# Performance work log

Measured on AMD Instinct MI355X. Metric: run time of the kernel, lower is better.

## Reference

```python
import jax, jax.numpy as jnp
import numpy as np
from jax import lax

N_LAYERS = 10  # Sinkhorn(n_layers=10)


def setup_inputs() -> dict:
    key = jax.random.key(0)
    k1, k2, k3 = jax.random.split(key, 3)
    S, NA, NB = 4, 4096, 4096
    alpha = jax.random.uniform(k1, (S, NA), jnp.float32, 0.05, 1.0)
    alpha = alpha / alpha.sum(-1, keepdims=True)  # probability simplex
    beta = jax.random.uniform(k2, (S, NB), jnp.float32, 0.05, 1.0)
    beta = beta / beta.sum(-1, keepdims=True)
    C = jax.random.uniform(k3, (NA, NB), jnp.float32)  # nonneg cost matrix
    eps = jnp.float32(0.1)  # entropic regularization
    return {"alpha": alpha, "beta": beta, "C": C, "eps": eps}


def reference(alpha, beta, C, eps):
    # Log-domain Sinkhorn: f,g are dual potentials, shapes (S,NA)/(S,NB).
    log_alpha = jnp.log(alpha)
    log_beta = jnp.log(beta)

    def log_dot_exp(A, b):
        # A: (n, m), b: (S, m) -> (S, n); matches torch log_dot_exp (2D case)
        return jax.scipy.special.logsumexp((-A[None, :, :] + b[:, None, :]) / eps, axis=-1)

    def step(carry, _):
        _, g = carry
        f = eps * (log_alpha - log_dot_exp(C, g))
        g = eps * (log_beta - log_dot_exp(C.T, f))
        return (f, g), None

    f0 = jnp.zeros_like(alpha)
    g0 = jnp.zeros_like(beta)
    (f, g), _ = lax.scan(step, (f0, g0), None, length=N_LAYERS)
    return f, g
```

## Files before the change

### kernel.cpp

```cpp
#include <hip/hip_runtime.h>
#include <stdint.h>

#define NN 4096
#define NITER 10
#define ROWS 16
#define NBLK 256
#define THREADS 512

#define RED_OFF 131072

typedef float v2f __attribute__((ext_vector_type(2)));

static __device__ __forceinline__ unsigned short f2bf(float f) {
  union { float f; unsigned int i; } x; x.f = f;
  unsigned int i = x.i;
  i += 0x7FFFu + ((i >> 16) & 1u);
  return (unsigned short)(i >> 16);
}
static __device__ __forceinline__ unsigned int pk2(float a, float b) {
  return (unsigned int)f2bf(a) | ((unsigned int)f2bf(b) << 16);
}
static __device__ __forceinline__ float2 unpk(unsigned int u) {
  union { unsigned int i; float f; } a, b;
  a.i = u << 16; b.i = u & 0xFFFF0000u;
  return make_float2(a.f, b.f);
}
static __device__ __forceinline__ float read_eps(const void* p) {
  float f = *(const float*)p;
  if (f > 1e-4f && f < 1.0f) return f;
  union { unsigned int i; float f; } x;
  x.i = ((unsigned int)*(const unsigned short*)p) << 16;
  return x.f;
}
static __device__ __forceinline__ void astore8(unsigned long long* p, unsigned long long v) {
  __hip_atomic_store(p, v, __ATOMIC_RELAXED, __HIP_MEMORY_SCOPE_AGENT);
}
static __device__ __forceinline__ v2f mk2(float a, float b) {
  v2f r; r.x = a; r.y = b; return r;
}
#define FMA2(a, b, c) __builtin_elementwise_fma(a, b, c)

__global__ __launch_bounds__(256) void zero_flags(unsigned int* __restrict__ c) {
#pragma unroll
  for (int k = 0; k < 32; ++k) c[threadIdx.x + k * 256] = 0;
}

static __device__ __forceinline__ void wait_group(
    const unsigned int* flags, int q, unsigned token) {
  const unsigned int* p = flags + (q * 64 + (threadIdx.x & 63)) * 16;
  for (int spin = 0; spin < 400000; ++spin) {
    unsigned v = __hip_atomic_load(p, __ATOMIC_RELAXED,
                                   __HIP_MEMORY_SCOPE_AGENT);
    if (__ballot(v >= token) == 0xFFFFFFFFFFFFFFFFull) break;
    __builtin_amdgcn_s_sleep(1);
  }
}

__global__ __launch_bounds__(THREADS, 1) void sinkhorn_all(
    const float* __restrict__ alpha, const float* __restrict__ beta,
    const float* __restrict__ C, const void* __restrict__ epsp,
    unsigned short* __restrict__ K, unsigned long long* __restrict__ u_ep,
    unsigned long long* __restrict__ v_ep, unsigned int* __restrict__ u_flags,
    unsigned int* __restrict__ v_flags, float* __restrict__ out) {
  __shared__ float4 smem4[8320];
  char* sm = (char*)smem4;
  const int t = threadIdx.x, b = blockIdx.x;
  const int wave = t >> 6, lane = t & 63;
  const int own = ((b & 7) << 5) | (b >> 3);
  const int base0 = own * ROWS;
  const float eps = read_eps(epsp);
  const float nie = -1.0f / eps;

#pragma unroll 2
  for (int r = 0; r < ROWS; ++r) {
    const float4* Crow = (const float4*)(C + (size_t)(base0 + r) * NN) + t * 2;
    float4 c0 = Crow[0], c1 = Crow[1];
    uint4 k0;
    k0.x = pk2(__expf(c0.x * nie), __expf(c0.y * nie));
    k0.y = pk2(__expf(c0.z * nie), __expf(c0.w * nie));
    k0.z = pk2(__expf(c1.x * nie), __expf(c1.y * nie));
    k0.w = pk2(__expf(c1.z * nie), __expf(c1.w * nie));
    ((uint4*)(K + (size_t)(base0 + r) * NN))[t] = k0;
  }

  {
    const int p = t & 3, cb = p * 4, rb = t >> 2;
#pragma unroll 1
    for (int q2 = 0; q2 < 32; q2 += 8) {
      float4 cv[8];
#pragma unroll
      for (int z = 0; z < 8; ++z)
        cv[z] = *(const float4*)(C + (size_t)((q2 + z) * 128 + rb) * NN + base0 + cb);
#pragma unroll
      for (int z = 0; z < 8; ++z) {
        int n = (q2 + z) * 128 + rb;
        int u16 = ((n >> 10) * 8 + ((n >> 3) & 7)) * 256 + ((n >> 6) & 15) * 16;
        int jo = (n & 7) * 2;
        *(unsigned short*)(sm + (size_t)(u16 + cb + 0) * 16 + jo) = f2bf(__expf(cv[z].x * nie));
        *(unsigned short*)(sm + (size_t)(u16 + cb + 1) * 16 + jo) = f2bf(__expf(cv[z].y * nie));
        *(unsigned short*)(sm + (size_t)(u16 + cb + 2) * 16 + jo) = f2bf(__expf(cv[z].z * nie));
        *(unsigned short*)(sm + (size_t)(u16 + cb + 3) * 16 + jo) = f2bf(__expf(cv[z].w * nie));
      }
    }
  }
  __syncthreads();

  const uint4* smu4 = (const uint4*)sm;
  const uint4 ONES = make_uint4(0x3F803F80u, 0x3F803F80u, 0x3F803F80u, 0x3F803F80u);

  for (int it = 0; it < NITER; ++it) {
    v2f acc01[2] = {}, acc23[2] = {};
    const int r0 = base0 + wave * 2;
    const uint4* Kr0 = (const uint4*)(K + (size_t)r0 * NN);
    const uint4* VB = (const uint4*)(v_ep + (size_t)(it - 1) * NN);
#pragma unroll 1
    for (int q = 0; q < 4; ++q) {
      if (it > 0) wait_group(v_flags, q, (unsigned)it);
#pragma unroll
      for (int ms = 0; ms < 2; ++ms) {
        const int fi = q * 128 + ms * 64 + lane;
        uint4 k0 = Kr0[fi], k1 = Kr0[512 + fi];
        uint4 svv[4];
        if (it == 0) {
          svv[0] = svv[1] = svv[2] = svv[3] = ONES;
        } else {
#pragma unroll
          for (int j = 0; j < 4; ++j) svv[j] = VB[fi * 4 + j];
        }
        unsigned cw0[4] = {k0.x, k0.y, k0.z, k0.w};
        unsigned cw1[4] = {k1.x, k1.y, k1.z, k1.w};
#pragma unroll
        for (int w = 0; w < 4; ++w) {
          float2 va = unpk(svv[w].x), vb_ = unpk(svv[w].y);
          float2 vc = unpk(svv[w].z), vd  = unpk(svv[w].w);
          float2 f0 = unpk(cw0[w]), f1 = unpk(cw1[w]);
          acc01[0] = FMA2(mk2(f0.x, f0.x), mk2(va.x, va.y), acc01[0]);
          acc23[0] = FMA2(mk2(f0.x, f0.x), mk2(vb_.x, vb_.y), acc23[0]);
          acc01[0] = FMA2(mk2(f0.y, f0.y), mk2(vc.x, vc.y), acc01[0]);
          acc23[0] = FMA2(mk2(f0.y, f0.y), mk2(vd.x, vd.y), acc23[0]);
          acc01[1] = FMA2(mk2(f1.x, f1.x), mk2(va.x, va.y), acc01[1]);
          acc23[1] = FMA2(mk2(f1.x, f1.x), mk2(vb_.x, vb_.y), acc23[1]);
          acc01[1] = FMA2(mk2(f1.y, f1.y), mk2(vc.x, vc.y), acc01[1]);
          acc23[1] = FMA2(mk2(f1.y, f1.y), mk2(vd.x, vd.y), acc23[1]);
        }
      }
    }
    {
      float accf[2][4];
#pragma unroll
      for (int rr = 0; rr < 2; ++rr) {
        accf[rr][0] = acc01[rr].x; accf[rr][1] = acc01[rr].y;
        accf[rr][2] = acc23[rr].x; accf[rr][3] = acc23[rr].y;
      }
#pragma unroll
      for (int off = 32; off > 0; off >>= 1)
#pragma unroll
        for (int rr = 0; rr < 2; ++rr)
#pragma unroll
          for (int s = 0; s < 4; ++s)
            accf[rr][s] += __shfl_xor(accf[rr][s], off);
      if (lane < 2) {
        int row = r0 + lane;
        float ux = alpha[0 * NN + row] / accf[lane][0];
        float uy = alpha[1 * NN + row] / accf[lane][1];
        float uz = alpha[2 * NN + row] / accf[lane][2];
        float uw = alpha[3 * NN + row] / accf[lane][3];
        unsigned long long ub = (unsigned long long)pk2(ux, uy) |
                                ((unsigned long long)pk2(uz, uw) << 32);
        astore8(u_ep + (size_t)it * NN + row, ub);
        if (it == NITER - 1) {
          out[0 * NN + row] = eps * __logf(ux);
          out[1 * NN + row] = eps * __logf(uy);
          out[2 * NN + row] = eps * __logf(uz);
          out[3 * NN + row] = eps * __logf(uw);
        }
      }
    }
    __syncthreads();
    if (t == 0)
      __hip_atomic_store(u_flags + own * 16, (unsigned)(it + 1),
                         __ATOMIC_RELAXED, __HIP_MEMORY_SCOPE_AGENT);

    const int cB = t & 7, k2n = (t >> 3) & 15, hB = t >> 7;
    const int kq = (hB * 1024 + k2n * 64) >> 1;
    wait_group(u_flags, hB, (unsigned)(it + 1));
    const uint4* UB = (const uint4*)(u_ep + (size_t)it * NN);
    v2f bacc01[2] = {}, bacc23[2] = {};
#pragma unroll
    for (int s = 0; s < 8; ++s) {
      uint4 kt0 = smu4[(hB * 8 + s) * 256 + k2n * 16 + cB];
      uint4 kt1 = smu4[(hB * 8 + s) * 256 + k2n * 16 + cB + 8];
      uint4 su[4];
#pragma unroll
      for (int j = 0; j < 4; ++j) su[j] = UB[kq + s * 4 + j];
      unsigned cw0[4] = {kt0.x, kt0.y, kt0.z, kt0.w};
      unsigned cw1[4] = {kt1.x, kt1.y, kt1.z, kt1.w};
#pragma unroll
      for (int w = 0; w < 4; ++w) {
        float2 ua = unpk(su[w].x), ub_ = unpk(su[w].y);
        float2 uc = unpk(su[w].z), ud  = unpk(su[w].w);
        float2 f0 = unpk(cw0[w]), f1 = unpk(cw1[w]);
        bacc01[0] = FMA2(mk2(f0.x, f0.x), mk2(ua.x, ua.y), bacc01[0]);
        bacc23[0] = FMA2(mk2(f0.x, f0.x), mk2(ub_.x, ub_.y), bacc23[0]);
        bacc01[0] = FMA2(mk2(f0.y, f0.y), mk2(uc.x, uc.y), bacc01[0]);
        bacc23[0] = FMA2(mk2(f0.y, f0.y), mk2(ud.x, ud.y), bacc23[0]);
        bacc01[1] = FMA2(mk2(f1.x, f1.x), mk2(ua.x, ua.y), bacc01[1]);
        bacc23[1] = FMA2(mk2(f1.x, f1.x), mk2(ub_.x, ub_.y), bacc23[1]);
        bacc01[1] = FMA2(mk2(f1.y, f1.y), mk2(uc.x, uc.y), bacc01[1]);
        bacc23[1] = FMA2(mk2(f1.y, f1.y), mk2(ud.x, ud.y), bacc23[1]);
      }
    }
    {
      float bf0[4] = {bacc01[0].x, bacc01[0].y, bacc23[0].x, bacc23[0].y};
      float bf1[4] = {bacc01[1].x, bacc01[1].y, bacc23[1].x, bacc23[1].y};
#pragma unroll
      for (int off = 8; off <= 32; off <<= 1)
#pragma unroll
        for (int s2 = 0; s2 < 4; ++s2) {
          bf0[s2] += __shfl_xor(bf0[s2], off);
          bf1[s2] += __shfl_xor(bf1[s2], off);
        }
      if (lane < 8) {
        float4* red = (float4*)(sm + RED_OFF);
        red[(wave * 8 + lane) * 2 + 0] = make_float4(bf0[0], bf0[1], bf0[2], bf0[3]);
        red[(wave * 8 + lane) * 2 + 1] = make_float4(bf1[0], bf1[1], bf1[2], bf1[3]);
      }
    }
    __syncthreads();
    if (t < 16) {
      const float4* red = (const float4*)(sm + RED_OFF);
      const int cc = t & 7, sel = t >> 3;
      float4 a = make_float4(0.f, 0.f, 0.f, 0.f);
#pragma unroll
      for (int g = 0; g < 8; ++g) {
        float4 r = red[(g * 8 + cc) * 2 + sel];
        a.x += r.x; a.y += r.y; a.z += r.z; a.w += r.w;
      }
      int m = base0 + t;
      float vx = beta[0 * NN + m] / a.x;
      float vy = beta[1 * NN + m] / a.y;
      float vz = beta[2 * NN + m] / a.z;
      float vw = beta[3 * NN + m] / a.w;
      unsigned long long vb = (unsigned long long)pk2(vx, vy) |
                              ((unsigned long long)pk2(vz, vw) << 32);
      astore8(v_ep + (size_t)it * NN + m, vb);
      if (it == NITER - 1) {
        out[4 * NN + 0 * NN + m] = eps * __logf(vx);
        out[4 * NN + 1 * NN + m] = eps * __logf(vy);
        out[4 * NN + 2 * NN + m] = eps * __logf(vz);
        out[4 * NN + 3 * NN + m] = eps * __logf(vw);
      }
    }
    __syncthreads();
    if (t == 0 && it < NITER - 1)
      __hip_atomic_store(v_flags + own * 16, (unsigned)(it + 1),
                         __ATOMIC_RELAXED, __HIP_MEMORY_SCOPE_AGENT);
  }
}

extern "C" void kernel_launch(void* const* d_in, const int* in_sizes, int n_in,
                              void* d_out, int out_size, void* d_ws, size_t ws_size,
                              hipStream_t stream) {
  (void)in_sizes; (void)n_in; (void)out_size; (void)ws_size;
  const float* alpha = (const float*)d_in[0];
  const float* beta  = (const float*)d_in[1];
  const float* C     = (const float*)d_in[2];
  const void*  epsp  = d_in[3];

  char* ws = (char*)d_ws;
  unsigned short* K        = (unsigned short*)ws;
  unsigned long long* u_ep = (unsigned long long*)(ws + 33554432);
  unsigned long long* v_ep = (unsigned long long*)(ws + 33554432 + 327680);
  unsigned int* u_flags    = (unsigned int*)(ws + 33554432 + 655360);
  unsigned int* v_flags    = (unsigned int*)(ws + 33554432 + 655360 + 16384);
  float* out = (float*)d_out;

  zero_flags<<<1, 256, 0, stream>>>(u_flags);
  sinkhorn_all<<<NBLK, THREADS, 0, stream>>>(alpha, beta, C, epsp, K,
                                             u_ep, v_ep, u_flags, v_flags, out);
}
```

Measured before the change: 250.0 us.

## Store scaling vectors in fp32, pack flags densely, prefetch K rows

Scaling vectors u and v are now exchanged between blocks as full fp32 instead of packed bf16, so the unpack work goes away and precision improves, at the cost of twice the exchange traffic. Flags are packed contiguously instead of padded to one per 64 bytes, which makes the polling loads more coalesced but may add false sharing. K row loads are software-prefetched one quarter ahead of the wait on v flags, so global latency overlaps the spin-wait. v at iteration zero is initialised to ones in a small prep kernel, which removes the it==0 branch.

```diff
diff --git a/kernel.cpp b/kernel.cpp
--- a/kernel.cpp
+++ b/kernel.cpp
@@ -8,6 +8,10 @@
 #define THREADS 512
 
 #define RED_OFF 131072
+
+#define U_EP_OFF 33554432
+#define V_EP_OFF 34209792
+#define FLAG_OFF 34930688
 
 typedef float v2f __attribute__((ext_vector_type(2)));
 
@@ -40,14 +44,19 @@
 }
 #define FMA2(a, b, c) __builtin_elementwise_fma(a, b, c)
 
-__global__ __launch_bounds__(256) void zero_flags(unsigned int* __restrict__ c) {
-#pragma unroll
-  for (int k = 0; k < 32; ++k) c[threadIdx.x + k * 256] = 0;
+__global__ __launch_bounds__(256) void init_ws(unsigned int* __restrict__ flags,
+                                               float* __restrict__ v0) {
+#pragma unroll
+  for (int k = 0; k < 32; ++k) flags[threadIdx.x + k * 256] = 0;
+  float4* p = (float4*)v0;
+#pragma unroll
+  for (int k = 0; k < 16; ++k)
+    p[threadIdx.x + k * 256] = make_float4(1.f, 1.f, 1.f, 1.f);
 }
 
 static __device__ __forceinline__ void wait_group(
     const unsigned int* flags, int q, unsigned token) {
-  const unsigned int* p = flags + (q * 64 + (threadIdx.x & 63)) * 16;
+  const unsigned int* p = flags + q * 64 + (threadIdx.x & 63);
   for (int spin = 0; spin < 400000; ++spin) {
     unsigned v = __hip_atomic_load(p, __ATOMIC_RELAXED,
                                    __HIP_MEMORY_SCOPE_AGENT);
@@ -59,8 +68,8 @@
 __global__ __launch_bounds__(THREADS, 1) void sinkhorn_all(
     const float* __restrict__ alpha, const float* __restrict__ beta,
     const float* __restrict__ C, const void* __restrict__ epsp,
-    unsigned short* __restrict__ K, unsigned long long* __restrict__ u_ep,
-    unsigned long long* __restrict__ v_ep, unsigned int* __restrict__ u_flags,
+    unsigned short* __restrict__ K, float* __restrict__ u_ep,
+    float* __restrict__ v_ep, unsigned int* __restrict__ u_flags,
     unsigned int* __restrict__ v_flags, float* __restrict__ out) {
   __shared__ float4 smem4[8320];
   char* sm = (char*)smem4;
@@ -106,43 +115,50 @@
   __syncthreads();
 
   const uint4* smu4 = (const uint4*)sm;
-  const uint4 ONES = make_uint4(0x3F803F80u, 0x3F803F80u, 0x3F803F80u, 0x3F803F80u);
 
   for (int it = 0; it < NITER; ++it) {
     v2f acc01[2] = {}, acc23[2] = {};
     const int r0 = base0 + wave * 2;
     const uint4* Kr0 = (const uint4*)(K + (size_t)r0 * NN);
-    const uint4* VB = (const uint4*)(v_ep + (size_t)(it - 1) * NN);
+    const float4* VB = (const float4*)v_ep + (size_t)it * NN;
+    uint4 ka[4];
+    ka[0] = Kr0[lane];       ka[1] = Kr0[512 + lane];
+    ka[2] = Kr0[64 + lane];  ka[3] = Kr0[576 + lane];
 #pragma unroll 1
     for (int q = 0; q < 4; ++q) {
+      uint4 kan[4];
+      if (q < 3) {
+        const int f = (q + 1) * 128 + lane;
+        kan[0] = Kr0[f];       kan[1] = Kr0[512 + f];
+        kan[2] = Kr0[64 + f];  kan[3] = Kr0[576 + f];
+      }
       if (it > 0) wait_group(v_flags, q, (unsigned)it);
 #pragma unroll
       for (int ms = 0; ms < 2; ++ms) {
         const int fi = q * 128 + ms * 64 + lane;
-        uint4 k0 = Kr0[fi], k1 = Kr0[512 + fi];
-        uint4 svv[4];
-        if (it == 0) {
-          svv[0] = svv[1] = svv[2] = svv[3] = ONES;
-        } else {
-#pragma unroll
-          for (int j = 0; j < 4; ++j) svv[j] = VB[fi * 4 + j];
-        }
+        float4 sv[8];
+#pragma unroll
+        for (int j = 0; j < 8; ++j) sv[j] = VB[fi * 8 + j];
+        const uint4 k0 = ka[ms * 2], k1 = ka[ms * 2 + 1];
         unsigned cw0[4] = {k0.x, k0.y, k0.z, k0.w};
         unsigned cw1[4] = {k1.x, k1.y, k1.z, k1.w};
 #pragma unroll
         for (int w = 0; w < 4; ++w) {
-          float2 va = unpk(svv[w].x), vb_ = unpk(svv[w].y);
-          float2 vc = unpk(svv[w].z), vd  = unpk(svv[w].w);
+          float4 e = sv[2 * w], o = sv[2 * w + 1];
           float2 f0 = unpk(cw0[w]), f1 = unpk(cw1[w]);
-          acc01[0] = FMA2(mk2(f0.x, f0.x), mk2(va.x, va.y), acc01[0]);
-          acc23[0] = FMA2(mk2(f0.x, f0.x), mk2(vb_.x, vb_.y), acc23[0]);
-          acc01[0] = FMA2(mk2(f0.y, f0.y), mk2(vc.x, vc.y), acc01[0]);
-          acc23[0] = FMA2(mk2(f0.y, f0.y), mk2(vd.x, vd.y), acc23[0]);
-          acc01[1] = FMA2(mk2(f1.x, f1.x), mk2(va.x, va.y), acc01[1]);
-          acc23[1] = FMA2(mk2(f1.x, f1.x), mk2(vb_.x, vb_.y), acc23[1]);
-          acc01[1] = FMA2(mk2(f1.y, f1.y), mk2(vc.x, vc.y), acc01[1]);
-          acc23[1] = FMA2(mk2(f1.y, f1.y), mk2(vd.x, vd.y), acc23[1]);
+          acc01[0] = FMA2(mk2(f0.x, f0.x), mk2(e.x, e.y), acc01[0]);
+          acc23[0] = FMA2(mk2(f0.x, f0.x), mk2(e.z, e.w), acc23[0]);
+          acc01[0] = FMA2(mk2(f0.y, f0.y), mk2(o.x, o.y), acc01[0]);
+          acc23[0] = FMA2(mk2(f0.y, f0.y), mk2(o.z, o.w), acc23[0]);
+          acc01[1] = FMA2(mk2(f1.x, f1.x), mk2(e.x, e.y), acc01[1]);
+          acc23[1] = FMA2(mk2(f1.x, f1.x), mk2(e.z, e.w), acc23[1]);
+          acc01[1] = FMA2(mk2(f1.y, f1.y), mk2(o.x, o.y), acc01[1]);
+          acc23[1] = FMA2(mk2(f1.y, f1.y), mk2(o.z, o.w), acc23[1]);
         }
+      }
+      if (q < 3) {
+#pragma unroll
+        for (int z = 0; z < 4; ++z) ka[z] = kan[z];
       }
     }
     {
@@ -165,9 +181,11 @@
         float uy = alpha[1 * NN + row] / accf[lane][1];
         float uz = alpha[2 * NN + row] / accf[lane][2];
         float uw = alpha[3 * NN + row] / accf[lane][3];
-        unsigned long long ub = (unsigned long long)pk2(ux, uy) |
-                                ((unsigned long long)pk2(uz, uw) << 32);
-        astore8(u_ep + (size_t)it * NN + row, ub);
+        union { float f[2]; unsigned long long u; } p0, p1;
+        p0.f[0] = ux; p0.f[1] = uy; p1.f[0] = uz; p1.f[1] = uw;
+        unsigned long long* dst =
+            (unsigned long long*)(u_ep + (size_t)it * NN * 4) + row * 2;
+        astore8(dst, p0.u); astore8(dst + 1, p1.u);
         if (it == NITER - 1) {
           out[0 * NN + row] = eps * __logf(ux);
           out[1 * NN + row] = eps * __logf(uy);
@@ -178,36 +196,35 @@
     }
     __syncthreads();
     if (t == 0)
-      __hip_atomic_store(u_flags + own * 16, (unsigned)(it + 1),
+      __hip_atomic_store(u_flags + own, (unsigned)(it + 1),
                          __ATOMIC_RELAXED, __HIP_MEMORY_SCOPE_AGENT);
 
     const int cB = t & 7, k2n = (t >> 3) & 15, hB = t >> 7;
-    const int kq = (hB * 1024 + k2n * 64) >> 1;
+    const int kbase = hB * 1024 + k2n * 64;
     wait_group(u_flags, hB, (unsigned)(it + 1));
-    const uint4* UB = (const uint4*)(u_ep + (size_t)it * NN);
+    const float4* UB = (const float4*)u_ep + (size_t)it * NN;
     v2f bacc01[2] = {}, bacc23[2] = {};
 #pragma unroll
     for (int s = 0; s < 8; ++s) {
       uint4 kt0 = smu4[(hB * 8 + s) * 256 + k2n * 16 + cB];
       uint4 kt1 = smu4[(hB * 8 + s) * 256 + k2n * 16 + cB + 8];
-      uint4 su[4];
-#pragma unroll
-      for (int j = 0; j < 4; ++j) su[j] = UB[kq + s * 4 + j];
+      float4 su[8];
+#pragma unroll
+      for (int j = 0; j < 8; ++j) su[j] = UB[kbase + s * 8 + j];
       unsigned cw0[4] = {kt0.x, kt0.y, kt0.z, kt0.w};
       unsigned cw1[4] = {kt1.x, kt1.y, kt1.z, kt1.w};
 #pragma unroll
       for (int w = 0; w < 4; ++w) {
-        float2 ua = unpk(su[w].x), ub_ = unpk(su[w].y);
-        float2 uc = unpk(su[w].z), ud  = unpk(su[w].w);
+        float4 e = su[2 * w], o = su[2 * w + 1];
         float2 f0 = unpk(cw0[w]), f1 = unpk(cw1[w]);
-        bacc01[0] = FMA2(mk2(f0.x, f0.x), mk2(ua.x, ua.y), bacc01[0]);
-        bacc23[0] = FMA2(mk2(f0.x, f0.x), mk2(ub_.x, ub_.y), bacc23[0]);
-        bacc01[0] = FMA2(mk2(f0.y, f0.y), mk2(uc.x, uc.y), bacc01[0]);
-        bacc23[0] = FMA2(mk2(f0.y, f0.y), mk2(ud.x, ud.y), bacc23[0]);
-        bacc01[1] = FMA2(mk2(f1.x, f1.x), mk2(ua.x, ua.y), bacc01[1]);
-        bacc23[1] = FMA2(mk2(f1.x, f1.x), mk2(ub_.x, ub_.y), bacc23[1]);
-        bacc01[1] = FMA2(mk2(f1.y, f1.y), mk2(uc.x, uc.y), bacc01[1]);
-        bacc23[1] = FMA2(mk2(f1.y, f1.y), mk2(ud.x, ud.y), bacc23[1]);
+        bacc01[0] = FMA2(mk2(f0.x, f0.x), mk2(e.x, e.y), bacc01[0]);
+        bacc23[0] = FMA2(mk2(f0.x, f0.x), mk2(e.z, e.w), bacc23[0]);
+        bacc01[0] = FMA2(mk2(f0.y, f0.y), mk2(o.x, o.y), bacc01[0]);
+        bacc23[0] = FMA2(mk2(f0.y, f0.y), mk2(o.z, o.w), bacc23[0]);
+        bacc01[1] = FMA2(mk2(f1.x, f1.x), mk2(e.x, e.y), bacc01[1]);
+        bacc23[1] = FMA2(mk2(f1.x, f1.x), mk2(e.z, e.w), bacc23[1]);
+        bacc01[1] = FMA2(mk2(f1.y, f1.y), mk2(o.x, o.y), bacc01[1]);
+        bacc23[1] = FMA2(mk2(f1.y, f1.y), mk2(o.z, o.w), bacc23[1]);
       }
     }
     {
@@ -241,9 +258,11 @@
       float vy = beta[1 * NN + m] / a.y;
       float vz = beta[2 * NN + m] / a.z;
       float vw = beta[3 * NN + m] / a.w;
-      unsigned long long vb = (unsigned long long)pk2(vx, vy) |
-                              ((unsigned long long)pk2(vz, vw) << 32);
-      astore8(v_ep + (size_t)it * NN + m, vb);
+      union { float f[2]; unsigned long long u; } p0, p1;
+      p0.f[0] = vx; p0.f[1] = vy; p1.f[0] = vz; p1.f[1] = vw;
+      unsigned long long* dst =
+          (unsigned long long*)(v_ep + (size_t)(it + 1) * NN * 4) + m * 2;
+      astore8(dst, p0.u); astore8(dst + 1, p1.u);
       if (it == NITER - 1) {
         out[4 * NN + 0 * NN + m] = eps * __logf(vx);
         out[4 * NN + 1 * NN + m] = eps * __logf(vy);
@@ -253,7 +272,7 @@
     }
     __syncthreads();
     if (t == 0 && it < NITER - 1)
-      __hip_atomic_store(v_flags + own * 16, (unsigned)(it + 1),
+      __hip_atomic_store(v_flags + own, (unsigned)(it + 1),
                          __ATOMIC_RELAXED, __HIP_MEMORY_SCOPE_AGENT);
   }
 }
@@ -268,14 +287,14 @@
   const void*  epsp  = d_in[3];
 
   char* ws = (char*)d_ws;
-  unsigned short* K        = (unsigned short*)ws;
-  unsigned long long* u_ep = (unsigned long long*)(ws + 33554432);
-  unsigned long long* v_ep = (unsigned long long*)(ws + 33554432 + 327680);
-  unsigned int* u_flags    = (unsigned int*)(ws + 33554432 + 655360);
-  unsigned int* v_flags    = (unsigned int*)(ws + 33554432 + 655360 + 16384);
+  unsigned short* K     = (unsigned short*)ws;
+  float* u_ep           = (float*)(ws + U_EP_OFF);
+  float* v_ep           = (float*)(ws + V_EP_OFF);
+  unsigned int* u_flags = (unsigned int*)(ws + FLAG_OFF);
+  unsigned int* v_flags = (unsigned int*)(ws + FLAG_OFF + 16384);
   float* out = (float*)d_out;
 
-  zero_flags<<<1, 256, 0, stream>>>(u_flags);
+  init_ws<<<1, 256, 0, stream>>>(u_flags, v_ep);
   sinkhorn_all<<<NBLK, THREADS, 0, stream>>>(alpha, beta, C, epsp, K,
                                              u_ep, v_ep, u_flags, v_flags, out);
 }
```

New measurement: 362.9 us. +45.2%, slower.

## Double block size to 1024 threads, halving per-thread rows and columns

Applied to the files above, without the earlier changes.

Raises the workgroup to 1024 threads so each wave handles one row in the u-update instead of two, and each thread covers half as many column groups in the v-update. The K precompute loops and the shared-memory reduction are remapped to the new thread count, and the reduction buffer is enlarged. The aim is more waves in flight per CU to hide global and LDS latency during the latency-bound Sinkhorn sweeps. In exchange it uses more registers per CU, adds cross-wave reduction work, and makes the per-block barriers more expensive.

```diff
diff --git a/kernel.cpp b/kernel.cpp
--- a/kernel.cpp
+++ b/kernel.cpp
@@ -5,7 +5,7 @@
 #define NITER 10
 #define ROWS 16
 #define NBLK 256
-#define THREADS 512
+#define THREADS 1024
 
 #define RED_OFF 131072
 
@@ -62,7 +62,7 @@
     unsigned short* __restrict__ K, unsigned long long* __restrict__ u_ep,
     unsigned long long* __restrict__ v_ep, unsigned int* __restrict__ u_flags,
     unsigned int* __restrict__ v_flags, float* __restrict__ out) {
-  __shared__ float4 smem4[8320];
+  __shared__ float4 smem4[8448];
   char* sm = (char*)smem4;
   const int t = threadIdx.x, b = blockIdx.x;
   const int wave = t >> 6, lane = t & 63;
@@ -72,28 +72,29 @@
   const float nie = -1.0f / eps;
 
 #pragma unroll 2
-  for (int r = 0; r < ROWS; ++r) {
-    const float4* Crow = (const float4*)(C + (size_t)(base0 + r) * NN) + t * 2;
+  for (int rp = 0; rp < 8; ++rp) {
+    const int r = rp * 2 + (t >> 9);
+    const float4* Crow = (const float4*)(C + (size_t)(base0 + r) * NN) + (t & 511) * 2;
     float4 c0 = Crow[0], c1 = Crow[1];
     uint4 k0;
     k0.x = pk2(__expf(c0.x * nie), __expf(c0.y * nie));
     k0.y = pk2(__expf(c0.z * nie), __expf(c0.w * nie));
     k0.z = pk2(__expf(c1.x * nie), __expf(c1.y * nie));
     k0.w = pk2(__expf(c1.z * nie), __expf(c1.w * nie));
-    ((uint4*)(K + (size_t)(base0 + r) * NN))[t] = k0;
+    ((uint4*)(K + (size_t)(base0 + r) * NN))[t & 511] = k0;
   }
 
   {
     const int p = t & 3, cb = p * 4, rb = t >> 2;
 #pragma unroll 1
-    for (int q2 = 0; q2 < 32; q2 += 8) {
+    for (int q2 = 0; q2 < 16; q2 += 8) {
       float4 cv[8];
 #pragma unroll
       for (int z = 0; z < 8; ++z)
-        cv[z] = *(const float4*)(C + (size_t)((q2 + z) * 128 + rb) * NN + base0 + cb);
+        cv[z] = *(const float4*)(C + (size_t)((q2 + z) * 256 + rb) * NN + base0 + cb);
 #pragma unroll
       for (int z = 0; z < 8; ++z) {
-        int n = (q2 + z) * 128 + rb;
+        int n = (q2 + z) * 256 + rb;
         int u16 = ((n >> 10) * 8 + ((n >> 3) & 7)) * 256 + ((n >> 6) & 15) * 16;
         int jo = (n & 7) * 2;
         *(unsigned short*)(sm + (size_t)(u16 + cb + 0) * 16 + jo) = f2bf(__expf(cv[z].x * nie));
@@ -109,8 +110,8 @@
   const uint4 ONES = make_uint4(0x3F803F80u, 0x3F803F80u, 0x3F803F80u, 0x3F803F80u);
 
   for (int it = 0; it < NITER; ++it) {
-    v2f acc01[2] = {}, acc23[2] = {};
-    const int r0 = base0 + wave * 2;
+    v2f acc01 = {}, acc23 = {};
+    const int r0 = base0 + wave;
     const uint4* Kr0 = (const uint4*)(K + (size_t)r0 * NN);
     const uint4* VB = (const uint4*)(v_ep + (size_t)(it - 1) * NN);
 #pragma unroll 1
@@ -119,7 +120,7 @@
 #pragma unroll
       for (int ms = 0; ms < 2; ++ms) {
         const int fi = q * 128 + ms * 64 + lane;
-        uint4 k0 = Kr0[fi], k1 = Kr0[512 + fi];
+        uint4 k0 = Kr0[fi];
         uint4 svv[4];
         if (it == 0) {
           svv[0] = svv[1] = svv[2] = svv[3] = ONES;
@@ -128,43 +129,31 @@
           for (int j = 0; j < 4; ++j) svv[j] = VB[fi * 4 + j];
         }
         unsigned cw0[4] = {k0.x, k0.y, k0.z, k0.w};
-        unsigned cw1[4] = {k1.x, k1.y, k1.z, k1.w};
 #pragma unroll
         for (int w = 0; w < 4; ++w) {
           float2 va = unpk(svv[w].x), vb_ = unpk(svv[w].y);
           float2 vc = unpk(svv[w].z), vd  = unpk(svv[w].w);
-          float2 f0 = unpk(cw0[w]), f1 = unpk(cw1[w]);
-          acc01[0] = FMA2(mk2(f0.x, f0.x), mk2(va.x, va.y), acc01[0]);
-          acc23[0] = FMA2(mk2(f0.x, f0.x), mk2(vb_.x, vb_.y), acc23[0]);
-          acc01[0] = FMA2(mk2(f0.y, f0.y), mk2(vc.x, vc.y), acc01[0]);
-          acc23[0] = FMA2(mk2(f0.y, f0.y), mk2(vd.x, vd.y), acc23[0]);
-          acc01[1] = FMA2(mk2(f1.x, f1.x), mk2(va.x, va.y), acc01[1]);
-          acc23[1] = FMA2(mk2(f1.x, f1.x), mk2(vb_.x, vb_.y), acc23[1]);
-          acc01[1] = FMA2(mk2(f1.y, f1.y), mk2(vc.x, vc.y), acc01[1]);
-          acc23[1] = FMA2(mk2(f1.y, f1.y), mk2(vd.x, vd.y), acc23[1]);
+          float2 f0 = unpk(cw0[w]);
+          acc01 = FMA2(mk2(f0.x, f0.x), mk2(va.x, va.y), acc01);
+          acc23 = FMA2(mk2(f0.x, f0.x), mk2(vb_.x, vb_.y), acc23);
+          acc01 = FMA2(mk2(f0.y, f0.y), mk2(vc.x, vc.y), acc01);
+          acc23 = FMA2(mk2(f0.y, f0.y), mk2(vd.x, vd.y), acc23);
         }
       }
     }
     {
-      float accf[2][4];
-#pragma unroll
-      for (int rr = 0; rr < 2; ++rr) {
-        accf[rr][0] = acc01[rr].x; accf[rr][1] = acc01[rr].y;
-        accf[rr][2] = acc23[rr].x; accf[rr][3] = acc23[rr].y;
-      }
+      float accf[4] = {acc01.x, acc01.y, acc23.x, acc23.y};
 #pragma unroll
       for (int off = 32; off > 0; off >>= 1)
 #pragma unroll
-        for (int rr = 0; rr < 2; ++rr)
-#pragma unroll
-          for (int s = 0; s < 4; ++s)
-            accf[rr][s] += __shfl_xor(accf[rr][s], off);
-      if (lane < 2) {
-        int row = r0 + lane;
-        float ux = alpha[0 * NN + row] / accf[lane][0];
-        float uy = alpha[1 * NN + row] / accf[lane][1];
-        float uz = alpha[2 * NN + row] / accf[lane][2];
-        float uw = alpha[3 * NN + row] / accf[lane][3];
+        for (int s = 0; s < 4; ++s)
+          accf[s] += __shfl_xor(accf[s], off);
+      if (lane == 0) {
+        int row = r0;
+        float ux = alpha[0 * NN + row] / accf[0];
+        float uy = alpha[1 * NN + row] / accf[1];
+        float uz = alpha[2 * NN + row] / accf[2];
+        float uw = alpha[3 * NN + row] / accf[3];
         unsigned long long ub = (unsigned long long)pk2(ux, uy) |
                                 ((unsigned long long)pk2(uz, uw) << 32);
         astore8(u_ep + (size_t)it * NN + row, ub);
@@ -181,15 +170,16 @@
       __hip_atomic_store(u_flags + own * 16, (unsigned)(it + 1),
                          __ATOMIC_RELAXED, __HIP_MEMORY_SCOPE_AGENT);
 
-    const int cB = t & 7, k2n = (t >> 3) & 15, hB = t >> 7;
-    const int kq = (hB * 1024 + k2n * 64) >> 1;
+    const int cB = t & 7, k2n = (t >> 3) & 31, hB = t >> 8;
+    const int k2 = k2n >> 1, gbase = hB * 8 + (k2n & 1) * 4;
+    const int kq = (hB * 1024 + k2 * 64 + (k2n & 1) * 32) >> 1;
     wait_group(u_flags, hB, (unsigned)(it + 1));
     const uint4* UB = (const uint4*)(u_ep + (size_t)it * NN);
     v2f bacc01[2] = {}, bacc23[2] = {};
 #pragma unroll
-    for (int s = 0; s < 8; ++s) {
-      uint4 kt0 = smu4[(hB * 8 + s) * 256 + k2n * 16 + cB];
-      uint4 kt1 = smu4[(hB * 8 + s) * 256 + k2n * 16 + cB + 8];
+    for (int s = 0; s < 4; ++s) {
+      uint4 kt0 = smu4[(gbase + s) * 256 + k2 * 16 + cB];
+      uint4 kt1 = smu4[(gbase + s) * 256 + k2 * 16 + cB + 8];
       uint4 su[4];
 #pragma unroll
       for (int j = 0; j < 4; ++j) su[j] = UB[kq + s * 4 + j];
@@ -232,7 +222,7 @@
       const int cc = t & 7, sel = t >> 3;
       float4 a = make_float4(0.f, 0.f, 0.f, 0.f);
 #pragma unroll
-      for (int g = 0; g < 8; ++g) {
+      for (int g = 0; g < 16; ++g) {
         float4 r = red[(g * 8 + cc) * 2 + sel];
         a.x += r.x; a.y += r.y; a.z += r.z; a.w += r.w;
       }
```

New measurement: 287.0 us. +14.8%, slower.
